# Optimization experiments

Measured on AMD Instinct MI355X. Metric: run time of the kernel, lower is better.

The kernel has to match this reference:

```python
import jax, jax.numpy as jnp
import numpy as np

NTASKS = 10
CAP = 3          # semantic_cap_size / num_capsules
SEQ = 128        # max_seq_length / class_dim
HID = 768
ADAPT = 2048
NEG = -10000.0
NUM_ITERS = 3


def squash(t, axis=-1):
    sq = jnp.sum(t * t, axis=axis, keepdims=True)
    return (sq / (1.0 + sq)) * t / jnp.sqrt(sq)


def setup_inputs() -> dict:
    key = jax.random.key(0)
    ks = jax.random.split(key, 12)
    B = 128
    sc = 0.02
    return {
        "x": jax.random.normal(ks[0], (B, SEQ, HID), jnp.float32),
        "t": 5,
        "s": jnp.ones((1,), jnp.float32),
        "fc1_w": jax.random.normal(ks[1], (ADAPT, HID), jnp.float32) * sc,
        "fc1_b": jnp.zeros((ADAPT,), jnp.float32),
        "fc2_w": jax.random.normal(ks[2], (HID, ADAPT), jnp.float32) * sc,
        "fc2_b": jnp.zeros((HID,), jnp.float32),
        "efc1": jax.random.normal(ks[3], (NTASKS, ADAPT), jnp.float32),
        "efc2": jax.random.normal(ks[4], (NTASKS, HID), jnp.float32),
        "sfc1_w": jax.random.normal(ks[5], (NTASKS, 100, HID), jnp.float32) * sc,
        "sfc1_b": jnp.zeros((NTASKS, 100), jnp.float32),
        "sfc2_w": jax.random.normal(ks[6], (NTASKS, CAP, 100), jnp.float32) * sc,
        "sfc2_b": jnp.zeros((NTASKS, CAP), jnp.float32),
        "route_weights": jax.random.normal(ks[7], (CAP, NTASKS, SEQ * CAP, SEQ), jnp.float32),
        "larger_w": jax.random.normal(ks[8], (HID, CAP), jnp.float32) * sc,
        "larger_b": jnp.zeros((HID,), jnp.float32),
        "elarger": jax.random.normal(ks[9], (NTASKS, HID), jnp.float32),
    }


def reference(x, t, s, fc1_w, fc1_b, fc2_w, fc2_b, efc1, efc2,
              sfc1_w, sfc1_b, sfc2_w, sfc2_b, route_weights,
              larger_w, larger_b, elarger):
    B = x.shape[0]
    # ---- semantic capsules: per-task two-layer linear (no activation) ----
    h1 = jnp.einsum('blh,nkh->nblk', x, sfc1_w) + sfc1_b[:, None, None, :]     # [N,B,L,100]
    sem = jnp.einsum('nblk,nck->nblc', h1, sfc2_w) + sfc2_b[:, None, None, :]  # [N,B,L,C]
    # torch: cat of per-task views [B, L*C, 1] along last dim -> [B, L*C, N]
    sem = jnp.transpose(sem, (1, 2, 3, 0)).reshape(B, SEQ * CAP, NTASKS)
    sem = squash(sem, axis=-1)                 # squash over task axis
    sem = jnp.transpose(sem, (0, 2, 1))        # [B, N, L*C]

    # ---- tsv capsules: dynamic routing-by-agreement ----
    # priors[c,b,n,0,l] = sum_d sem[b,n,d] * route_weights[c,n,d,l]
    priors = jnp.einsum('bnd,cndl->cbnl', sem, route_weights)[:, :, :, None, :]  # [C,B,N,1,L]
    tsv = jnp.tril(jnp.ones((NTASKS, NTASKS), x.dtype))
    tsv_row = tsv[t].reshape(1, 1, NTASKS, 1, 1)                                  # [1,1,N,1,1]
    route_mask = jnp.where(tsv_row == 0, jnp.asarray(NEG, x.dtype), 0.0)

    logits = jnp.zeros_like(priors)
    vote_outputs = None
    for i in range(NUM_ITERS):
        logits = logits * tsv_row + route_mask
        probs = jax.nn.softmax(logits, axis=2)
        vote_outputs = jnp.sum(probs * priors, axis=2, keepdims=True)  # [C,B,1,1,L]
        outputs = squash(vote_outputs, axis=-1)
        if i != NUM_ITERS - 1:
            logits = logits + jnp.sum(priors * outputs, axis=-1, keepdims=True)

    # torch .view(B, L, -1) on contiguous [C,B,1,1,L] (row-major reshape)
    h_out = vote_outputs.reshape(B, SEQ, CAP)
    h_out = h_out @ larger_w.T + larger_b                       # [B,L,HID]
    glarger = jax.nn.sigmoid(s * elarger[t])                    # [HID]
    capsule_output = h_out * glarger

    # ---- masked adapter over (x + capsule_output) ----
    h = x + capsule_output
    gfc1 = jax.nn.sigmoid(s * efc1[t])
    gfc2 = jax.nn.sigmoid(s * efc2[t])
    h = jax.nn.relu(h @ fc1_w.T + fc1_b) * gfc1
    h = jax.nn.relu(h @ fc2_w.T + fc2_b) * gfc2
    return x + h
```

## Files before the change

kernel.cpp:

```cpp
#include <hip/hip_runtime.h>
#include <hip/hip_bf16.h>
#include <math.h>
#include <stdint.h>

typedef __bf16 bf16;
typedef __bf16 bf16x8 __attribute__((ext_vector_type(8)));
typedef __bf16 bf16x4 __attribute__((ext_vector_type(4)));
typedef float  f32x4  __attribute__((ext_vector_type(4)));

#define NTASKS 10
#define CAP    3
#define SEQ    128
#define HID    768
#define ADAPT  2048
#define BATCH  128
#define BL     (BATCH*SEQ)
#define NEGV   (-10000.0f)

__device__ __forceinline__ float sigmoidf_(float z) { return 1.f / (1.f + expf(-z)); }

__device__ __forceinline__ void gld16(const void* g, void* l) {
    auto gp = (const __attribute__((address_space(1))) uint32_t*)g;
    auto lp = (__attribute__((address_space(3))) uint32_t*)(uint32_t)(uintptr_t)l;
    __builtin_amdgcn_global_load_lds(gp, lp, 16, 0, 0);
}

__global__ void k_gates(const float* efc1, const float* efc2, const float* elarger,
                        const float* s, const int* tptr,
                        float* gfc1, float* gfc2, float* glarger) {
    int i = blockIdx.x * 256 + threadIdx.x;
    int t = *tptr; float sv = *s;
    if (i < ADAPT)                gfc1[i] = sigmoidf_(sv * efc1[t * ADAPT + i]);
    else if (i < ADAPT + HID)     { int j = i - ADAPT;        gfc2[j]    = sigmoidf_(sv * efc2[t * HID + j]); }
    else if (i < ADAPT + 2 * HID) { int j = i - ADAPT - HID;  glarger[j] = sigmoidf_(sv * elarger[t * HID + j]); }
}

__global__ void k_fusew(const float* sfc1_w, const float* sfc1_b,
                        const float* sfc2_w, const float* sfc2_b,
                        bf16* Wb, float* bb) {
    int j = blockIdx.x;
    int n = j / CAP;
    if (j >= 30) {
        for (int i = threadIdx.x; i < HID; i += 256) Wb[j * HID + i] = (bf16)0.f;
        if (threadIdx.x == 0) bb[j] = 0.f;
        return;
    }
    __shared__ float w2[100];
    if (threadIdx.x < 100) w2[threadIdx.x] = sfc2_w[j * 100 + threadIdx.x];
    __syncthreads();
    const float* w1 = sfc1_w + (size_t)n * 100 * HID;
    float a0 = 0, a1 = 0, a2 = 0;
    for (int k = 0; k < 100; ++k) {
        float s2 = w2[k];
        const float* r = w1 + k * HID;
        a0 += s2 * r[threadIdx.x];
        a1 += s2 * r[threadIdx.x + 256];
        a2 += s2 * r[threadIdx.x + 512];
    }
    Wb[j * HID + threadIdx.x]       = (bf16)a0;
    Wb[j * HID + threadIdx.x + 256] = (bf16)a1;
    Wb[j * HID + threadIdx.x + 512] = (bf16)a2;
    if (threadIdx.x == 0) {
        float b = sfc2_b[j];
        for (int k = 0; k < 100; ++k) b += sfc1_b[n * 100 + k] * w2[k];
        bb[j] = b;
    }
}

__global__ void k_convert(const float* fc1_w, const float* fc2_w, bf16* B1, bf16* B2) {
    int i = blockIdx.x * 256 + threadIdx.x;
    const int quarter = ADAPT * HID / 4;
    if (i < quarter) {
        float4 v = ((const float4*)fc1_w)[i];
        bf16x4 o = { (bf16)v.x, (bf16)v.y, (bf16)v.z, (bf16)v.w };
        ((bf16x4*)B1)[i] = o;
    } else if (i < 2 * quarter) {
        int j = i - quarter;
        float4 v = ((const float4*)fc2_w)[j];
        bf16x4 o = { (bf16)v.x, (bf16)v.y, (bf16)v.z, (bf16)v.w };
        ((bf16x4*)B2)[j] = o;
    }
}

__global__ void k_rwT(const float* __restrict__ rw, bf16* __restrict__ rwb) {
    int cn = blockIdx.x;
    int d0 = blockIdx.y * 64;
    __shared__ float t[64][129];
    const float* src = rw + (size_t)cn * 384 * 128;
    int tid = threadIdx.x;
    #pragma unroll
    for (int p = 0; p < 8; ++p) {
        int f4 = tid + p * 256;
        int row = f4 >> 5, c4 = (f4 & 31) * 4;
        float4 v = *(const float4*)(src + (size_t)(d0 + row) * 128 + c4);
        t[row][c4] = v.x; t[row][c4 + 1] = v.y; t[row][c4 + 2] = v.z; t[row][c4 + 3] = v.w;
    }
    __syncthreads();
    bf16* dst = rwb + (size_t)cn * 128 * 384 + d0;
    #pragma unroll
    for (int p = 0; p < 4; ++p) {
        int i8 = tid + p * 256;
        int l = i8 >> 3, d8 = (i8 & 7) * 8;
        bf16x8 o;
        #pragma unroll
        for (int i = 0; i < 8; ++i) o[i] = (bf16)t[d8 + i][l];
        *(bf16x8*)(dst + (size_t)l * 384 + d8) = o;
    }
}

__launch_bounds__(256)
__global__ void k_semg(const float* __restrict__ x, const bf16* __restrict__ Wb,
                       const float* __restrict__ bb, bf16* __restrict__ semb) {
    __shared__ __align__(16) bf16 As[64 * 32];
    __shared__ __align__(16) bf16 Bs[32 * 32];
    __shared__ float sem_s[64][33];
    const int tid = threadIdx.x;
    const int wave = tid >> 6, lane = tid & 63;
    const int tm = blockIdx.x;
    const int lr = lane & 15, kg = (lane >> 4) * 8;
    f32x4 acc[2] = {};

    const float* xbase = x + (size_t)(tm * 64 + (tid >> 2)) * HID + (tid & 3) * 8;
    const bf16* wbase = Wb + (size_t)(tid >> 2) * HID + (tid & 3) * 8;
    bf16* BsW = Bs + wave * 512;

    for (int k0 = 0; k0 < HID; k0 += 32) {
        float xv[8];
        *(float4*)&xv[0] = *(const float4*)(xbase + k0);
        *(float4*)&xv[4] = *(const float4*)(xbase + k0 + 4);
        __syncthreads();
        if (tid < 128) gld16(wbase + k0, BsW);
        bf16x8 xb;
        #pragma unroll
        for (int i = 0; i < 8; ++i) xb[i] = (bf16)xv[i];
        *(bf16x8*)&As[tid * 8] = xb;
        __syncthreads();
        bf16x8 af = *(const bf16x8*)&As[(wave * 16 + lr) * 32 + kg];
        bf16x8 b0 = *(const bf16x8*)&Bs[lr * 32 + kg];
        bf16x8 b1 = *(const bf16x8*)&Bs[(16 + lr) * 32 + kg];
        acc[0] = __builtin_amdgcn_mfma_f32_16x16x32_bf16(af, b0, acc[0], 0, 0, 0);
        acc[1] = __builtin_amdgcn_mfma_f32_16x16x32_bf16(af, b1, acc[1], 0, 0, 0);
    }

    #pragma unroll
    for (int n = 0; n < 2; ++n) {
        int col = n * 16 + lr;
        float bv = bb[col];
        #pragma unroll
        for (int r = 0; r < 4; ++r) {
            int row = wave * 16 + (lane >> 4) * 4 + r;
            sem_s[row][col] = acc[n][r] + bv;
        }
    }
    __syncthreads();
    if (tid < 64) {
        int bl = tm * 64 + tid;
        int b = bl >> 7, l = bl & 127;
        float vals[30];
        float sq[3] = {0.f, 0.f, 0.f};
        #pragma unroll
        for (int j = 0; j < 30; ++j) { float v = sem_s[tid][j]; vals[j] = v; sq[j % 3] += v * v; }
        float scl[3];
        #pragma unroll
        for (int c = 0; c < 3; ++c) scl[c] = (sq[c] / (1.f + sq[c])) / sqrtf(sq[c]);
        #pragma unroll
        for (int j = 0; j < 30; ++j)
            semb[((size_t)(j / 3) * BATCH + b) * 384 + l * 3 + (j % 3)] = (bf16)(vals[j] * scl[j % 3]);
    }
}

__launch_bounds__(256)
__global__ void k_priorsG(const bf16* __restrict__ semb, const bf16* __restrict__ rwb,
                          float* __restrict__ priors) {
    __shared__ __align__(16) bf16 As[128 * 32];
    __shared__ __align__(16) bf16 Bs[128 * 32];
    const int cn = blockIdx.x;
    const int c = cn / NTASKS, n = cn % NTASKS;
    const int tid = threadIdx.x;
    const int wave = tid >> 6, lane = tid & 63;
    const int wr = wave >> 1, wc = wave & 1;
    const int lr = lane & 15, kg = (lane >> 4) * 8;
    const int K = 384;
    f32x4 acc[4][4] = {};

    const bf16* Abase = semb + ((size_t)n * BATCH + (tid >> 2)) * K + (tid & 3) * 8;
    const bf16* Bbase = rwb + ((size_t)cn * 128 + (tid >> 2)) * K + (tid & 3) * 8;
    bf16* AsW = As + wave * 512;
    bf16* BsW = Bs + wave * 512;

    for (int k0 = 0; k0 < K; k0 += 32) {
        __syncthreads();
        gld16(Abase + k0, AsW);
        gld16(Abase + k0 + (size_t)64 * K, AsW + 2048);
        gld16(Bbase + k0, BsW);
        gld16(Bbase + k0 + (size_t)64 * K, BsW + 2048);
        __syncthreads();
        bf16x8 af[4], bfr[4];
        #pragma unroll
        for (int m = 0; m < 4; ++m)
            af[m] = *(const bf16x8*)&As[(wr * 64 + m * 16 + lr) * 32 + kg];
        #pragma unroll
        for (int nn = 0; nn < 4; ++nn)
            bfr[nn] = *(const bf16x8*)&Bs[(wc * 64 + nn * 16 + lr) * 32 + kg];
        #pragma unroll
        for (int m = 0; m < 4; ++m)
            #pragma unroll
            for (int nn = 0; nn < 4; ++nn)
                acc[m][nn] = __builtin_amdgcn_mfma_f32_16x16x32_bf16(af[m], bfr[nn], acc[m][nn], 0, 0, 0);
    }

    #pragma unroll
    for (int nn = 0; nn < 4; ++nn) {
        int col = wc * 64 + nn * 16 + lr;
        #pragma unroll
        for (int m = 0; m < 4; ++m) {
            int row0 = wr * 64 + m * 16 + (lane >> 4) * 4;
            #pragma unroll
            for (int r = 0; r < 4; ++r) {
                int row = row0 + r;
                priors[(((size_t)c * BATCH + row) * NTASKS + n) * 128 + col] = acc[m][nn][r];
            }
        }
    }
}

__global__ void k_routing(const float* __restrict__ priors, const int* tptr,
                          float* __restrict__ vote) {
    int cb = blockIdx.x;
    int lane = threadIdx.x;
    int t = *tptr;
    float p0[NTASKS], p1[NTASKS], ln[NTASKS];
    const float* pb = priors + (size_t)cb * NTASKS * 128;
    #pragma unroll
    for (int n = 0; n < NTASKS; ++n) {
        p0[n] = pb[n * 128 + lane];
        p1[n] = pb[n * 128 + 64 + lane];
        ln[n] = 0.f;
    }
    float v0 = 0.f, v1 = 0.f;
    for (int it = 0; it < 3; ++it) {
        float lm[NTASKS];
        float mx = -3.4e38f;
        #pragma unroll
        for (int n = 0; n < NTASKS; ++n) { lm[n] = (n <= t) ? ln[n] : NEGV; mx = fmaxf(mx, lm[n]); }
        float e[NTASKS], se = 0.f;
        #pragma unroll
        for (int n = 0; n < NTASKS; ++n) { e[n] = expf(lm[n] - mx); se += e[n]; }
        float inv = 1.f / se;
        v0 = 0.f; v1 = 0.f;
        #pragma unroll
        for (int n = 0; n < NTASKS; ++n) { float pr = e[n] * inv; v0 += pr * p0[n]; v1 += pr * p1[n]; }
        if (it == 2) break;
        float sq = v0 * v0 + v1 * v1;
        #pragma unroll
        for (int m = 32; m >= 1; m >>= 1) sq += __shfl_xor(sq, m);
        float scale = (sq / (1.f + sq)) / sqrtf(sq);
        float o0 = v0 * scale, o1 = v1 * scale;
        #pragma unroll
        for (int n = 0; n < NTASKS; ++n) {
            float d = p0[n] * o0 + p1[n] * o1;
            #pragma unroll
            for (int m = 32; m >= 1; m >>= 1) d += __shfl_xor(d, m);
            ln[n] = lm[n] + d;
        }
    }
    vote[(size_t)cb * 128 + lane]      = v0;
    vote[(size_t)cb * 128 + 64 + lane] = v1;
}

__global__ void k_buildH(const float* __restrict__ x, const float* __restrict__ vote,
                         const float* __restrict__ lw, const float* __restrict__ lb,
                         const float* __restrict__ glarger, bf16* __restrict__ H) {
    int idx = blockIdx.x * 256 + threadIdx.x;
    int bl = idx / 192, h4 = (idx % 192) * 4;
    float v0 = vote[bl * 3 + 0], v1 = vote[bl * 3 + 1], v2 = vote[bl * 3 + 2];
    float xa[4];
    *(float4*)xa = ((const float4*)x)[idx];
    bf16x4 o;
    #pragma unroll
    for (int r = 0; r < 4; ++r) {
        int hid = h4 + r;
        float hv = v0 * lw[hid * 3] + v1 * lw[hid * 3 + 1] + v2 * lw[hid * 3 + 2] + lb[hid];
        o[r] = (bf16)(xa[r] + hv * glarger[hid]);
    }
    ((bf16x4*)H)[idx] = o;
}

template <int MODE>
__launch_bounds__(512, 4)
__global__ void k_gemmW(const bf16* __restrict__ A, const bf16* __restrict__ Bw,
                        const float* __restrict__ bias, const float* __restrict__ gate,
                        const float* __restrict__ X, void* __restrict__ Out,
                        int K, int N, int TN, int NT) {
    __shared__ __align__(16) char smem[49152];
    const int tid = threadIdx.x;
    const int lane = tid & 63, w = tid >> 6;
    const int lr = lane & 15, kq = lane >> 4;
    const int qr = w >> 2, qc = w & 3;
    const int nwg = gridDim.x, bid = blockIdx.x;
    const int cpx = nwg >> 3;
    const int wg = (bid & 7) * cpx + (bid >> 3);
    const int tm = wg / TN, tn = wg % TN;

    const int srow = lane >> 2;
    const int schunk = (lane & 3) ^ ((lane >> 3) & 3);
    const bf16* Ab  = A  + (size_t)(tm * 128 + w * 16 + srow) * K + schunk * 8;
    const bf16* Bb0 = Bw + (size_t)(tn * 256 + w * 16 + srow) * K + schunk * 8;
    const bf16* Bb1 = Bb0 + (size_t)128 * K;
    auto As_ = [&](int buf) { return smem + buf * 8192; };
    auto Bs_ = [&](int buf) { return smem + 16384 + buf * 16384; };
    auto stage = [&](int k0, int buf) {
        gld16(Ab  + k0, As_(buf) + w * 1024);
        gld16(Bb0 + k0, Bs_(buf) + w * 1024);
        gld16(Bb1 + k0, Bs_(buf) + 8192 + w * 1024);
    };

    const int psw = (lr >> 1) & 3;
    f32x4 acc[4][4] = {};
    bf16x8 a[4], b[4];

    stage(0, 0);
    asm volatile("s_waitcnt vmcnt(0)" ::: "memory");
    __builtin_amdgcn_s_barrier();

    for (int T = 0; T < NT; ++T) {
        const int buf = T & 1;
        const bool more = (T + 1 < NT);
        if (more) stage((T + 1) * 32, buf ^ 1);
        const char* ab = As_(buf);
        const char* bb = Bs_(buf);
        #pragma unroll
        for (int m = 0; m < 4; ++m)
            a[m] = *(const bf16x8*)(ab + (qr * 64 + m * 16 + lr) * 64 + ((kq ^ psw) << 4));
        #pragma unroll
        for (int n = 0; n < 4; ++n)
            b[n] = *(const bf16x8*)(bb + (qc * 64 + n * 16 + lr) * 64 + ((kq ^ psw) << 4));
        asm volatile("s_waitcnt lgkmcnt(0)" ::: "memory");
        __builtin_amdgcn_sched_barrier(0);
        __builtin_amdgcn_s_setprio(1);
        #pragma unroll
        for (int m = 0; m < 4; ++m)
            #pragma unroll
            for (int n = 0; n < 4; ++n)
                acc[m][n] = __builtin_amdgcn_mfma_f32_16x16x32_bf16(a[m], b[n], acc[m][n], 0, 0, 0);
        __builtin_amdgcn_s_setprio(0);
        if (more) asm volatile("s_waitcnt vmcnt(0)" ::: "memory");
        __builtin_amdgcn_s_barrier();
    }

    #pragma unroll
    for (int n = 0; n < 4; ++n) {
        int col = tn * 256 + qc * 64 + n * 16 + lr;
        float bv = bias[col], gv = gate[col];
        #pragma unroll
        for (int m = 0; m < 4; ++m) {
            int row0 = tm * 128 + qr * 64 + m * 16 + kq * 4;
            #pragma unroll
            for (int r = 0; r < 4; ++r) {
                float v = fmaxf(acc[m][n][r] + bv, 0.f) * gv;
                int row = row0 + r;
                if (MODE == 1) {
                    ((bf16*)Out)[(size_t)row * N + col] = (bf16)v;
                } else {
                    size_t o = (size_t)row * HID + col;
                    ((float*)Out)[o] = X[o] + v;
                }
            }
        }
    }
}

extern "C" void kernel_launch(void* const* d_in, const int* in_sizes, int n_in,
                              void* d_out, int out_size, void* d_ws, size_t ws_size,
                              hipStream_t stream) {
    const float* x      = (const float*)d_in[0];
    const int*   t      = (const int*)  d_in[1];
    const float* s      = (const float*)d_in[2];
    const float* fc1_w  = (const float*)d_in[3];
    const float* fc1_b  = (const float*)d_in[4];
    const float* fc2_w  = (const float*)d_in[5];
    const float* fc2_b  = (const float*)d_in[6];
    const float* efc1   = (const float*)d_in[7];
    const float* efc2   = (const float*)d_in[8];
    const float* sfc1_w = (const float*)d_in[9];
    const float* sfc1_b = (const float*)d_in[10];
    const float* sfc2_w = (const float*)d_in[11];
    const float* sfc2_b = (const float*)d_in[12];
    const float* rw     = (const float*)d_in[13];
    const float* lw     = (const float*)d_in[14];
    const float* lb     = (const float*)d_in[15];
    const float* elarger= (const float*)d_in[16];

    char* ws = (char*)d_ws;
    size_t off = 0;
    auto alloc = [&](size_t b) { void* p = ws + off; off = (off + b + 255) & ~(size_t)255; return p; };
    float* gfc1    = (float*)alloc(ADAPT * 4);
    float* gfc2    = (float*)alloc(HID * 4);
    float* glarger = (float*)alloc(HID * 4);
    bf16*  Wb      = (bf16*) alloc(32 * HID * 2);
    float* bb      = (float*)alloc(32 * 4);
    bf16*  B1      = (bf16*) alloc((size_t)ADAPT * HID * 2);
    bf16*  B2      = (bf16*) alloc((size_t)ADAPT * HID * 2);
    bf16*  semb    = (bf16*) alloc((size_t)NTASKS * BATCH * 384 * 2);
    bf16*  rwb     = (bf16*) alloc((size_t)30 * 128 * 384 * 2);
    float* priors  = (float*)alloc((size_t)CAP * BATCH * NTASKS * 128 * 4);
    float* vote    = (float*)alloc((size_t)CAP * BATCH * 128 * 4);
    bf16*  H1      = (bf16*) alloc((size_t)BL * ADAPT * 2);
    bf16*  H       = (bf16*)d_out;

    k_gates  <<<14, 256, 0, stream>>>(efc1, efc2, elarger, s, t, gfc1, gfc2, glarger);
    k_fusew  <<<32, 256, 0, stream>>>(sfc1_w, sfc1_b, sfc2_w, sfc2_b, Wb, bb);
    k_convert<<<3072, 256, 0, stream>>>(fc1_w, fc2_w, B1, B2);
    k_rwT    <<<dim3(30, 6), 256, 0, stream>>>(rw, rwb);
    k_semg   <<<BL / 64, 256, 0, stream>>>(x, Wb, bb, semb);
    k_priorsG<<<30, 256, 0, stream>>>(semb, rwb, priors);
    k_routing<<<CAP * BATCH, 64, 0, stream>>>(priors, t, vote);
    k_buildH <<<BL * 192 / 256, 256, 0, stream>>>(x, vote, lw, lb, glarger, H);
    k_gemmW<1><<<1024, 512, 0, stream>>>(H,  B1, fc1_b, gfc1, nullptr, H1,   HID,   ADAPT, 8, HID / 32);
    k_gemmW<2><<<384, 512, 0, stream>>>(H1, B2, fc2_b, gfc2, x,       d_out, ADAPT, HID,  3, ADAPT / 32);
}
```

Measured before the change: 199.0 us.

## Deepen GEMM pipeline to six LDS stages with register double-buffering

Replaces the double-buffered LDS pipeline in the adapter GEMMs with a six-slot ring that prefetches five K-tiles ahead. Fragment loads for the next tile are issued before the current tile's MFMAs, so LDS reads overlap compute. This hides more global-load latency and avoids waiting on all loads every step. In exchange it uses 144KB of LDS per block and drops occupancy to two blocks per CU, which may cut latency hiding between waves.

```diff
diff --git a/kernel.cpp b/kernel.cpp
--- a/kernel.cpp
+++ b/kernel.cpp
@@ -287,12 +287,12 @@
 }
 
 template <int MODE>
-__launch_bounds__(512, 4)
-__global__ void k_gemmW(const bf16* __restrict__ A, const bf16* __restrict__ Bw,
+__launch_bounds__(512, 2)
+__global__ void k_gemmP(const bf16* __restrict__ A, const bf16* __restrict__ Bw,
                         const float* __restrict__ bias, const float* __restrict__ gate,
                         const float* __restrict__ X, void* __restrict__ Out,
                         int K, int N, int TN, int NT) {
-    __shared__ __align__(16) char smem[49152];
+    __shared__ __align__(16) char smem[147456];
     const int tid = threadIdx.x;
     const int lane = tid & 63, w = tid >> 6;
     const int lr = lane & 15, kq = lane >> 4;
@@ -307,46 +307,71 @@
     const bf16* Ab  = A  + (size_t)(tm * 128 + w * 16 + srow) * K + schunk * 8;
     const bf16* Bb0 = Bw + (size_t)(tn * 256 + w * 16 + srow) * K + schunk * 8;
     const bf16* Bb1 = Bb0 + (size_t)128 * K;
-    auto As_ = [&](int buf) { return smem + buf * 8192; };
-    auto Bs_ = [&](int buf) { return smem + 16384 + buf * 16384; };
+    auto As_ = [&](int buf) { return smem + buf * 24576; };
+    auto Bs_ = [&](int buf) { return smem + buf * 24576 + 8192; };
     auto stage = [&](int k0, int buf) {
         gld16(Ab  + k0, As_(buf) + w * 1024);
         gld16(Bb0 + k0, Bs_(buf) + w * 1024);
         gld16(Bb1 + k0, Bs_(buf) + 8192 + w * 1024);
     };
 
-    const int psw = (lr >> 1) & 3;
+    const int rsl = (kq ^ ((lr >> 1) & 3)) << 4;
     f32x4 acc[4][4] = {};
-    bf16x8 a[4], b[4];
-
-    stage(0, 0);
-    asm volatile("s_waitcnt vmcnt(0)" ::: "memory");
+    bf16x8 aA[4], bA[4], aB[4], bB[4];
+
+    for (int i = 0; i < 5 && i < NT; ++i) stage(i * 32, i);
+    if (NT > 4)      asm volatile("s_waitcnt vmcnt(9)" ::: "memory");
+    else if (NT > 3) asm volatile("s_waitcnt vmcnt(6)" ::: "memory");
+    else if (NT > 2) asm volatile("s_waitcnt vmcnt(3)" ::: "memory");
+    else             asm volatile("s_waitcnt vmcnt(0)" ::: "memory");
     __builtin_amdgcn_s_barrier();
-
-    for (int T = 0; T < NT; ++T) {
-        const int buf = T & 1;
-        const bool more = (T + 1 < NT);
-        if (more) stage((T + 1) * 32, buf ^ 1);
-        const char* ab = As_(buf);
-        const char* bb = Bs_(buf);
-        #pragma unroll
-        for (int m = 0; m < 4; ++m)
-            a[m] = *(const bf16x8*)(ab + (qr * 64 + m * 16 + lr) * 64 + ((kq ^ psw) << 4));
-        #pragma unroll
-        for (int n = 0; n < 4; ++n)
-            b[n] = *(const bf16x8*)(bb + (qc * 64 + n * 16 + lr) * 64 + ((kq ^ psw) << 4));
-        asm volatile("s_waitcnt lgkmcnt(0)" ::: "memory");
-        __builtin_amdgcn_sched_barrier(0);
-        __builtin_amdgcn_s_setprio(1);
-        #pragma unroll
-        for (int m = 0; m < 4; ++m)
-            #pragma unroll
-            for (int n = 0; n < 4; ++n)
-                acc[m][n] = __builtin_amdgcn_mfma_f32_16x16x32_bf16(a[m], b[n], acc[m][n], 0, 0, 0);
-        __builtin_amdgcn_s_setprio(0);
-        if (more) asm volatile("s_waitcnt vmcnt(0)" ::: "memory");
-        __builtin_amdgcn_s_barrier();
-    }
+    {
+        const char* ab = As_(0); const char* bb = Bs_(0);
+        #pragma unroll
+        for (int m = 0; m < 4; ++m) aA[m] = *(const bf16x8*)(ab + (qr * 64 + m * 16 + lr) * 64 + rsl);
+        #pragma unroll
+        for (int n = 0; n < 4; ++n) bA[n] = *(const bf16x8*)(bb + (qc * 64 + n * 16 + lr) * 64 + rsl);
+    }
+
+#define TILE_STEP(T, ACUR, BCUR, ANXT, BNXT)                                      \
+    {                                                                             \
+        const int t_ = (T);                                                       \
+        if (t_ + 1 < NT) {                                                        \
+            const char* ab = As_((t_ + 1) % 6);                                   \
+            const char* bb = Bs_((t_ + 1) % 6);                                   \
+            _Pragma("unroll")                                                     \
+            for (int m = 0; m < 4; ++m)                                           \
+                ANXT[m] = *(const bf16x8*)(ab + (qr * 64 + m * 16 + lr) * 64 + rsl); \
+            _Pragma("unroll")                                                     \
+            for (int n = 0; n < 4; ++n)                                           \
+                BNXT[n] = *(const bf16x8*)(bb + (qc * 64 + n * 16 + lr) * 64 + rsl); \
+            asm volatile("s_waitcnt lgkmcnt(8)" ::: "memory");                    \
+        } else {                                                                  \
+            asm volatile("s_waitcnt lgkmcnt(0)" ::: "memory");                    \
+        }                                                                         \
+        __builtin_amdgcn_sched_barrier(0);                                        \
+        __builtin_amdgcn_s_setprio(1);                                            \
+        _Pragma("unroll")                                                         \
+        for (int m = 0; m < 4; ++m)                                               \
+            _Pragma("unroll")                                                     \
+            for (int n = 0; n < 4; ++n)                                           \
+                acc[m][n] = __builtin_amdgcn_mfma_f32_16x16x32_bf16(              \
+                    ACUR[m], BCUR[n], acc[m][n], 0, 0, 0);                        \
+        __builtin_amdgcn_s_setprio(0);                                            \
+        __builtin_amdgcn_sched_barrier(0);                                        \
+        if (t_ + 5 < NT) stage((t_ + 5) * 32, (t_ + 5) % 6);                      \
+        if (t_ + 5 < NT)      asm volatile("s_waitcnt vmcnt(9)" ::: "memory");    \
+        else if (t_ + 4 < NT) asm volatile("s_waitcnt vmcnt(6)" ::: "memory");    \
+        else if (t_ + 3 < NT) asm volatile("s_waitcnt vmcnt(3)" ::: "memory");    \
+        else                  asm volatile("s_waitcnt vmcnt(0)" ::: "memory");    \
+        __builtin_amdgcn_s_barrier();                                             \
+    }
+
+    for (int T = 0; T < NT; T += 2) {
+        TILE_STEP(T,     aA, bA, aB, bB);
+        TILE_STEP(T + 1, aB, bB, aA, bA);
+    }
+#undef TILE_STEP
 
     #pragma unroll
     for (int n = 0; n < 4; ++n) {
@@ -416,6 +441,6 @@
     k_priorsG<<<30, 256, 0, stream>>>(semb, rwb, priors);
     k_routing<<<CAP * BATCH, 64, 0, stream>>>(priors, t, vote);
     k_buildH <<<BL * 192 / 256, 256, 0, stream>>>(x, vote, lw, lb, glarger, H);
-    k_gemmW<1><<<1024, 512, 0, stream>>>(H,  B1, fc1_b, gfc1, nullptr, H1,   HID,   ADAPT, 8, HID / 32);
-    k_gemmW<2><<<384, 512, 0, stream>>>(H1, B2, fc2_b, gfc2, x,       d_out, ADAPT, HID,  3, ADAPT / 32);
-}
+    k_gemmP<1><<<1024, 512, 0, stream>>>(H,  B1, fc1_b, gfc1, nullptr, H1,   HID,   ADAPT, 8, HID / 32);
+    k_gemmP<2><<<384, 512, 0, stream>>>(H1, B2, fc2_b, gfc2, x,       d_out, ADAPT, HID,  3, ADAPT / 32);
+}
```

Measured after the change: 222.6 us. +11.9%, slower.
